# Kernel optimization log

Measured on AMD Instinct MI355X. Metric: run time of the kernel, lower is better.

Reference implementation:

```python
import jax, jax.numpy as jnp
import numpy as np

B, C, L = 1, 256, 1024      # batch, channels, seq_length
WIN, FEAT = 80, 256          # window_size, feature_size


def setup_inputs() -> dict:
    key = jax.random.key(0)
    ks = jax.random.split(key, 9)
    s = 0.02
    return {
        "x":  jax.random.normal(ks[0], (B, C, L), dtype=jnp.float32),
        # weights stored as [in, out] (transpose of torch Linear.weight)
        "Wq": jax.random.normal(ks[1], (WIN, FEAT), dtype=jnp.float32) * s,
        "bq": jax.random.normal(ks[2], (FEAT,), dtype=jnp.float32) * s,
        "Wk": jax.random.normal(ks[3], (WIN, FEAT), dtype=jnp.float32) * s,
        "bk": jax.random.normal(ks[4], (FEAT,), dtype=jnp.float32) * s,
        "Wv": jax.random.normal(ks[5], (WIN, FEAT), dtype=jnp.float32) * s,
        "bv": jax.random.normal(ks[6], (FEAT,), dtype=jnp.float32) * s,
        "Wf": jax.random.normal(ks[7], (FEAT, C), dtype=jnp.float32) * s,
        "bf": jax.random.normal(ks[8], (C,), dtype=jnp.float32) * s,
    }


def reference(x, Wq, bq, Wk, bk, Wv, bv, Wf, bf):
    Bb, Cc, Ll = x.shape
    half = WIN // 2
    # fixed-width window per position, clamped to stay in-bounds
    starts = jnp.clip(jnp.arange(Ll) - half, 0, Ll - WIN)          # [L]
    idx = starts[:, None] + jnp.arange(WIN)                        # [L, W]
    win = x[:, :, idx]                                             # [B, C, L, W]
    win = win.transpose(0, 2, 1, 3)                                # [B, L, C, W]
    q = win @ Wq + bq                                              # [B, L, C, F]
    k = win @ Wk + bk                                              # [B, L, C, F]
    v = win @ Wv + bv                                              # [B, L, C, F]
    scores = jax.nn.softmax(jnp.einsum('blcf,bldf->blcd', q, k), axis=-1)  # [B,L,C,C]
    attn = jnp.einsum('blcd,bldf->blcf', scores, v)                # [B, L, C, F]
    pooled = attn.mean(axis=2)                                     # [B, L, F] (mean over channels)
    out = pooled @ Wf + bf                                         # [B, L, C]
    return out.transpose(0, 2, 1)                                  # [B, C, L]
```

## Files before the change

### kernel.cpp

```cpp
#include <hip/hip_runtime.h>

#define Lc    1024
#define Cc    256
#define WINc  80
#define SLOTS 96
#define RS    88
#define L2E   1.44269504088896340736f

typedef __attribute__((ext_vector_type(8)))  short bf16x8;
typedef __attribute__((ext_vector_type(16))) float f32x16;
typedef __attribute__((ext_vector_type(4)))  unsigned int u32x4;

__device__ inline float bf2f(unsigned short h) { return __uint_as_float(((unsigned int)h) << 16); }
__device__ inline unsigned int cvt_pk_bf16(float lo, float hi) {
    unsigned int r;
    asm("v_cvt_pk_bf16_f32 %0, %1, %2" : "=v"(r) : "v"(lo), "v"(hi));
    return r;
}
__device__ inline unsigned short f2bf(float f) {
    unsigned int u = __float_as_uint(f);
    unsigned int r = u + 0x7FFFu + ((u >> 16) & 1u);
    return (unsigned short)(r >> 16);
}

__global__ __launch_bounds__(256) void precompute_kernel(
    const float* __restrict__ Wq, const float* __restrict__ bq,
    const float* __restrict__ Wk, const float* __restrict__ Wv,
    const float* __restrict__ bv, const float* __restrict__ Wf,
    const float* __restrict__ bf,
    unsigned short* __restrict__ Gt, float* __restrict__ WvWf,
    float* __restrict__ bias3)
{
    const int b = blockIdx.x;
    const int t = threadIdx.x;
    if (b < SLOTS) {
        if (t < WINc) {
            const int s = b;
            const int k = (s & ~12) | ((s & 4) << 1) | ((s & 8) >> 1);
            float acc = 0.f;
            if (k < WINc) {
                for (int f = 0; f < 256; ++f)
                    acc = fmaf(Wq[t * 256 + f], Wk[k * 256 + f], acc);
            } else if (k == WINc) {
                for (int f = 0; f < 256; ++f)
                    acc = fmaf(bq[f], Wk[t * 256 + f], acc);
            }
            Gt[s * WINc + t] = (k <= WINc) ? f2bf(acc * L2E) : (unsigned short)0;
        }
    } else if (b < SLOTS + WINc) {
        const int w = b - SLOTS;
        float acc = 0.f;
        for (int f = 0; f < 256; ++f)
            acc = fmaf(Wv[w * 256 + f], Wf[f * 256 + t], acc);
        WvWf[w * 256 + t] = acc * (1.0f / 256.0f);
    } else {
        float acc = bf[t];
        for (int f = 0; f < 256; ++f)
            acc = fmaf(bv[f], Wf[f * 256 + t], acc);
        bias3[t] = acc;
    }
}

__global__ __launch_bounds__(512, 2) void local_attn_kernel(
    const float* __restrict__ x,
    const unsigned short* __restrict__ Gt_ws,
    const float* __restrict__ WvWf, const float* __restrict__ bias3,
    float* __restrict__ out)
{
    __shared__ __align__(16) unsigned short winb[Cc * RS];
    __shared__ __align__(16) unsigned short Gtb[SLOTS * RS];
    __shared__ float sbeta[Cc];
    __shared__ float sbarAcc[Cc];
    __shared__ float ubuf[WINc];
    __shared__ float scratch[8 * Cc];

    const int l = blockIdx.x;
    int s0 = l - WINc / 2;
    s0 = s0 < 0 ? 0 : (s0 > (Lc - WINc) ? (Lc - WINc) : s0);
    const int tid  = threadIdx.x;
    const int lane = tid & 63;
    const int wid  = tid >> 6;
    const int ln31 = lane & 31;
    const int hh   = lane >> 5;

    for (int i = tid; i < Cc * WINc / 8; i += 512) {
        const int c  = i & 255;
        const int ch = i >> 8;
        const float* xp = &x[c * Lc + s0 + ch * 8];
        union { u32x4 u; bf16x8 v; } pk;
        pk.u.x = cvt_pk_bf16(xp[0], xp[1]);
        pk.u.y = cvt_pk_bf16(xp[2], xp[3]);
        pk.u.z = cvt_pk_bf16(xp[4], xp[5]);
        pk.u.w = cvt_pk_bf16(xp[6], xp[7]);
        *(bf16x8*)&winb[c * RS + ch * 8] = pk.v;
    }
    for (int i = tid; i < SLOTS * WINc / 2; i += 512) {
        const int s = i / 40;
        const int j = i - s * 40;
        ((unsigned int*)Gtb)[s * (RS / 2) + j] = ((const unsigned int*)Gt_ws)[i];
    }
    __syncthreads();

    f32x16 tt[3];
    {
        bf16x8 bfr[5];
        #pragma unroll
        for (int t = 0; t < 5; ++t)
            bfr[t] = *(const bf16x8*)&winb[(wid * 32 + ln31) * RS + t * 16 + hh * 8];
        #pragma unroll
        for (int mt = 0; mt < 3; ++mt) {
            f32x16 a;
            #pragma unroll
            for (int r = 0; r < 16; ++r) a[r] = 0.f;
            #pragma unroll
            for (int t = 0; t < 5; ++t) {
                bf16x8 afr = *(const bf16x8*)&Gtb[(mt * 32 + ln31) * RS + t * 16 + hh * 8];
                a = __builtin_amdgcn_mfma_f32_32x32x16_bf16(afr, bfr[t], a, 0, 0, 0);
            }
            tt[mt] = a;
        }
    }
    if (hh == 0) sbeta[wid * 32 + ln31] = tt[2][8];

    bf16x8 af[5];
    #pragma unroll
    for (int t = 0; t < 5; ++t) {
        const int m = t >> 1, o = 8 * (t & 1);
        union { u32x4 u; bf16x8 v; } pk;
        pk.u.x = cvt_pk_bf16(tt[m][o + 0], tt[m][o + 1]);
        pk.u.y = cvt_pk_bf16(tt[m][o + 2], tt[m][o + 3]);
        pk.u.z = cvt_pk_bf16(tt[m][o + 4], tt[m][o + 5]);
        pk.u.w = cvt_pk_bf16(tt[m][o + 6], tt[m][o + 7]);
        af[t] = pk.v;
    }

    f32x16 acc[8];
    #pragma unroll
    for (int nt = 0; nt < 8; ++nt) {
        f32x16 a;
        #pragma unroll
        for (int r = 0; r < 16; ++r) a[r] = 0.f;
        #pragma unroll
        for (int t = 0; t < 5; ++t) {
            bf16x8 b = *(const bf16x8*)&winb[(nt * 32 + ln31) * RS + t * 16 + hh * 8];
            a = __builtin_amdgcn_mfma_f32_32x32x16_bf16(af[t], b, a, 0, 0, 0);
        }
        acc[nt] = a;
    }
    __syncthreads();

    float zp[16];
    #pragma unroll
    for (int r = 0; r < 16; ++r) zp[r] = 0.f;
    #pragma unroll
    for (int nt = 0; nt < 8; ++nt) {
        const float sb = sbeta[nt * 32 + ln31];
        #pragma unroll
        for (int r = 0; r < 16; ++r) {
            const float e = exp2f(acc[nt][r] + sb);
            acc[nt][r] = e;
            zp[r] += e;
        }
    }
    #pragma unroll
    for (int r = 0; r < 16; ++r) {
        float z = zp[r];
        z += __shfl_xor(z, 1);
        z += __shfl_xor(z, 2);
        z += __shfl_xor(z, 4);
        z += __shfl_xor(z, 8);
        z += __shfl_xor(z, 16);
        zp[r] = __builtin_amdgcn_rcpf(z);
    }

    #pragma unroll
    for (int nt = 0; nt < 8; ++nt) {
        float v = 0.f;
        #pragma unroll
        for (int r = 0; r < 16; ++r) v = fmaf(acc[nt][r], zp[r], v);
        v += __shfl_xor(v, 32);
        if (lane < 32) scratch[wid * Cc + nt * 32 + ln31] = v;
    }
    __syncthreads();

    if (tid < Cc) {
        float v = 0.f;
        #pragma unroll
        for (int w8 = 0; w8 < 8; ++w8) v += scratch[w8 * Cc + tid];
        sbarAcc[tid] = v;
    }
    __syncthreads();

    if (tid < 4 * WINc) {
        const int w = tid % WINc;
        const int part = tid / WINc;
        const int d0 = part * 64;
        float a = 0.f;
        #pragma unroll 8
        for (int d = d0; d < d0 + 64; ++d)
            a = fmaf(sbarAcc[d], bf2f(winb[d * RS + w]), a);
        scratch[part * WINc + w] = a;
    }
    __syncthreads();
    if (tid < WINc)
        ubuf[tid] = scratch[tid] + scratch[WINc + tid] +
                    scratch[2 * WINc + tid] + scratch[3 * WINc + tid];
    __syncthreads();

    {
        const int co = tid & 255;
        const int part = tid >> 8;
        const int w0 = part * 40;
        float a = 0.f;
        #pragma unroll 8
        for (int w = w0; w < w0 + 40; ++w)
            a = fmaf(ubuf[w], WvWf[w * 256 + co], a);
        scratch[part * 256 + co] = a;
    }
    __syncthreads();
    if (tid < Cc)
        out[tid * Lc + l] = scratch[tid] + scratch[256 + tid] + bias3[tid];
}

extern "C" void kernel_launch(void* const* d_in, const int* in_sizes, int n_in,
                              void* d_out, int out_size, void* d_ws, size_t ws_size,
                              hipStream_t stream)
{
    const float* x  = (const float*)d_in[0];
    const float* Wq = (const float*)d_in[1];
    const float* bq = (const float*)d_in[2];
    const float* Wk = (const float*)d_in[3];
    const float* Wv = (const float*)d_in[5];
    const float* bv = (const float*)d_in[6];
    const float* Wf = (const float*)d_in[7];
    const float* bf = (const float*)d_in[8];
    float* out = (float*)d_out;

    unsigned short* Gt = (unsigned short*)d_ws;
    float* WvWf  = (float*)((char*)d_ws + SLOTS * WINc * 2);
    float* bias3 = WvWf + WINc * 256;

    hipLaunchKernelGGL(precompute_kernel, dim3(SLOTS + WINc + 1), dim3(256), 0, stream,
                       Wq, bq, Wk, Wv, bv, Wf, bf, Gt, WvWf, bias3);
    hipLaunchKernelGGL(local_attn_kernel, dim3(Lc), dim3(512), 0, stream,
                       x, Gt, WvWf, bias3, out);
}
```

Before: 72.08 us.

## Process two adjacent positions per block sharing one widened window tile

Each block now handles two consecutive sequence positions. It loads a single 81-wide window (padded to 96 columns) that covers both, and uses two shifted Gram tables precomputed for offsets 0 and 1. Gram tiles are read directly from global memory instead of being staged in LDS. The softmax/pooling epilogues of the two positions are interleaved to share barriers. This halves the window loads and launches, at the cost of a sixth MFMA k-step, doubled accumulator registers, and more global reads of the Gram table.

```diff
diff --git a/kernel.cpp b/kernel.cpp
--- a/kernel.cpp
+++ b/kernel.cpp
@@ -1,11 +1,12 @@
 #include <hip/hip_runtime.h>
 
-#define Lc    1024
-#define Cc    256
-#define WINc  80
-#define SLOTS 96
-#define RS    88
-#define L2E   1.44269504088896340736f
+#define Lc     1024
+#define Cc     256
+#define WINc   80
+#define SLOTS  96
+#define RS     104
+#define GSTRIDE 96
+#define L2E    1.44269504088896340736f
 
 typedef __attribute__((ext_vector_type(8)))  short bf16x8;
 typedef __attribute__((ext_vector_type(16))) float f32x16;
@@ -33,22 +34,28 @@
 {
     const int b = blockIdx.x;
     const int t = threadIdx.x;
-    if (b < SLOTS) {
-        if (t < WINc) {
-            const int s = b;
-            const int k = (s & ~12) | ((s & 4) << 1) | ((s & 8) >> 1);
-            float acc = 0.f;
-            if (k < WINc) {
+    if (b < 2 * SLOTS) {
+        if (t >= SLOTS) return;
+        const int dl = b / SLOTS;
+        const int s  = b % SLOTS;
+        const int j  = (s & ~12) | ((s & 4) << 1) | ((s & 8) >> 1);
+        const int i  = t;
+        float acc = 0.f;
+        bool nz = false;
+        if (j == 81) {
+            if (i >= dl && i - dl < WINc) {
+                nz = true;
                 for (int f = 0; f < 256; ++f)
-                    acc = fmaf(Wq[t * 256 + f], Wk[k * 256 + f], acc);
-            } else if (k == WINc) {
-                for (int f = 0; f < 256; ++f)
-                    acc = fmaf(bq[f], Wk[t * 256 + f], acc);
+                    acc = fmaf(bq[f], Wk[(i - dl) * 256 + f], acc);
             }
-            Gt[s * WINc + t] = (k <= WINc) ? f2bf(acc * L2E) : (unsigned short)0;
-        }
-    } else if (b < SLOTS + WINc) {
-        const int w = b - SLOTS;
+        } else if (j < 81 && j >= dl && j - dl < WINc && i >= dl && i - dl < WINc) {
+            nz = true;
+            for (int f = 0; f < 256; ++f)
+                acc = fmaf(Wq[(i - dl) * 256 + f], Wk[(j - dl) * 256 + f], acc);
+        }
+        Gt[dl * SLOTS * GSTRIDE + s * GSTRIDE + i] = nz ? f2bf(acc * L2E) : (unsigned short)0;
+    } else if (b < 2 * SLOTS + WINc) {
+        const int w = b - 2 * SLOTS;
         float acc = 0.f;
         for (int f = 0; f < 256; ++f)
             acc = fmaf(Wv[w * 256 + f], Wf[f * 256 + t], acc);
@@ -61,70 +68,26 @@
     }
 }
 
-__global__ __launch_bounds__(512, 2) void local_attn_kernel(
-    const float* __restrict__ x,
-    const unsigned short* __restrict__ Gt_ws,
-    const float* __restrict__ WvWf, const float* __restrict__ bias3,
-    float* __restrict__ out)
-{
-    __shared__ __align__(16) unsigned short winb[Cc * RS];
-    __shared__ __align__(16) unsigned short Gtb[SLOTS * RS];
-    __shared__ float sbeta[Cc];
-    __shared__ float sbarAcc[Cc];
-    __shared__ float ubuf[WINc];
-    __shared__ float scratch[8 * Cc];
-
-    const int l = blockIdx.x;
-    int s0 = l - WINc / 2;
-    s0 = s0 < 0 ? 0 : (s0 > (Lc - WINc) ? (Lc - WINc) : s0);
-    const int tid  = threadIdx.x;
-    const int lane = tid & 63;
-    const int wid  = tid >> 6;
-    const int ln31 = lane & 31;
-    const int hh   = lane >> 5;
-
-    for (int i = tid; i < Cc * WINc / 8; i += 512) {
-        const int c  = i & 255;
-        const int ch = i >> 8;
-        const float* xp = &x[c * Lc + s0 + ch * 8];
-        union { u32x4 u; bf16x8 v; } pk;
-        pk.u.x = cvt_pk_bf16(xp[0], xp[1]);
-        pk.u.y = cvt_pk_bf16(xp[2], xp[3]);
-        pk.u.z = cvt_pk_bf16(xp[4], xp[5]);
-        pk.u.w = cvt_pk_bf16(xp[6], xp[7]);
-        *(bf16x8*)&winb[c * RS + ch * 8] = pk.v;
-    }
-    for (int i = tid; i < SLOTS * WINc / 2; i += 512) {
-        const int s = i / 40;
-        const int j = i - s * 40;
-        ((unsigned int*)Gtb)[s * (RS / 2) + j] = ((const unsigned int*)Gt_ws)[i];
-    }
-    __syncthreads();
-
+__device__ inline void make_af(const unsigned short* __restrict__ Gtab,
+                               const bf16x8 bwin[6], float* sbeta_buf,
+                               bf16x8 af[6], int wid, int ln31, int hh)
+{
     f32x16 tt[3];
-    {
-        bf16x8 bfr[5];
-        #pragma unroll
-        for (int t = 0; t < 5; ++t)
-            bfr[t] = *(const bf16x8*)&winb[(wid * 32 + ln31) * RS + t * 16 + hh * 8];
-        #pragma unroll
-        for (int mt = 0; mt < 3; ++mt) {
-            f32x16 a;
-            #pragma unroll
-            for (int r = 0; r < 16; ++r) a[r] = 0.f;
-            #pragma unroll
-            for (int t = 0; t < 5; ++t) {
-                bf16x8 afr = *(const bf16x8*)&Gtb[(mt * 32 + ln31) * RS + t * 16 + hh * 8];
-                a = __builtin_amdgcn_mfma_f32_32x32x16_bf16(afr, bfr[t], a, 0, 0, 0);
-            }
-            tt[mt] = a;
-        }
-    }
-    if (hh == 0) sbeta[wid * 32 + ln31] = tt[2][8];
-
-    bf16x8 af[5];
-    #pragma unroll
-    for (int t = 0; t < 5; ++t) {
+    #pragma unroll
+    for (int mt = 0; mt < 3; ++mt) {
+        f32x16 a;
+        #pragma unroll
+        for (int r = 0; r < 16; ++r) a[r] = 0.f;
+        #pragma unroll
+        for (int t = 0; t < 6; ++t) {
+            bf16x8 g = *(const bf16x8*)&Gtab[(mt * 32 + ln31) * GSTRIDE + t * 16 + hh * 8];
+            a = __builtin_amdgcn_mfma_f32_32x32x16_bf16(g, bwin[t], a, 0, 0, 0);
+        }
+        tt[mt] = a;
+    }
+    if (hh == 0) sbeta_buf[wid * 32 + ln31] = tt[2][9];
+    #pragma unroll
+    for (int t = 0; t < 6; ++t) {
         const int m = t >> 1, o = 8 * (t & 1);
         union { u32x4 u; bf16x8 v; } pk;
         pk.u.x = cvt_pk_bf16(tt[m][o + 0], tt[m][o + 1]);
@@ -133,28 +96,18 @@
         pk.u.w = cvt_pk_bf16(tt[m][o + 6], tt[m][o + 7]);
         af[t] = pk.v;
     }
-
-    f32x16 acc[8];
+}
+
+__device__ inline void softmax_colpart(f32x16 acc[8], const float* sbeta_buf,
+                                       float* colpart, int wid, int lane)
+{
+    const int ln31 = lane & 31;
+    float zp[16];
+    #pragma unroll
+    for (int r = 0; r < 16; ++r) zp[r] = 0.f;
     #pragma unroll
     for (int nt = 0; nt < 8; ++nt) {
-        f32x16 a;
-        #pragma unroll
-        for (int r = 0; r < 16; ++r) a[r] = 0.f;
-        #pragma unroll
-        for (int t = 0; t < 5; ++t) {
-            bf16x8 b = *(const bf16x8*)&winb[(nt * 32 + ln31) * RS + t * 16 + hh * 8];
-            a = __builtin_amdgcn_mfma_f32_32x32x16_bf16(af[t], b, a, 0, 0, 0);
-        }
-        acc[nt] = a;
-    }
-    __syncthreads();
-
-    float zp[16];
-    #pragma unroll
-    for (int r = 0; r < 16; ++r) zp[r] = 0.f;
-    #pragma unroll
-    for (int nt = 0; nt < 8; ++nt) {
-        const float sb = sbeta[nt * 32 + ln31];
+        const float sb = sbeta_buf[nt * 32 + ln31];
         #pragma unroll
         for (int r = 0; r < 16; ++r) {
             const float e = exp2f(acc[nt][r] + sb);
@@ -172,25 +125,100 @@
         z += __shfl_xor(z, 16);
         zp[r] = __builtin_amdgcn_rcpf(z);
     }
-
     #pragma unroll
     for (int nt = 0; nt < 8; ++nt) {
         float v = 0.f;
         #pragma unroll
         for (int r = 0; r < 16; ++r) v = fmaf(acc[nt][r], zp[r], v);
         v += __shfl_xor(v, 32);
-        if (lane < 32) scratch[wid * Cc + nt * 32 + ln31] = v;
-    }
+        if (lane < 32) colpart[wid * Cc + nt * 32 + ln31] = v;
+    }
+}
+
+__global__ __launch_bounds__(512, 2) void local_attn_kernel(
+    const float* __restrict__ x,
+    const unsigned short* __restrict__ Gt,
+    const float* __restrict__ WvWf, const float* __restrict__ bias3,
+    float* __restrict__ out)
+{
+    __shared__ __align__(16) unsigned short winb[Cc * RS];
+    __shared__ float sbeta0[Cc], sbeta1[Cc];
+    __shared__ float colpart[8 * Cc];
+    __shared__ float sbarAcc[Cc];
+    __shared__ float upart[4 * WINc];
+    __shared__ float ubuf[WINc];
+    __shared__ float outpart[2 * Cc];
+
+    const int bid = blockIdx.x;
+    const int lA = 2 * bid, lB = lA + 1;
+    int sA = lA - WINc / 2; sA = sA < 0 ? 0 : (sA > (Lc - WINc) ? (Lc - WINc) : sA);
+    int sB = lB - WINc / 2; sB = sB < 0 ? 0 : (sB > (Lc - WINc) ? (Lc - WINc) : sB);
+    const int dB = sB - sA;
+
+    const int tid  = threadIdx.x;
+    const int lane = tid & 63;
+    const int wid  = tid >> 6;
+    const int ln31 = lane & 31;
+    const int hh   = lane >> 5;
+
+    for (int i = tid; i < Cc * 12; i += 512) {
+        const int c  = i / 12;
+        const int ch = i - c * 12;
+        union { u32x4 u; bf16x8 v; } pk;
+        if (ch < 10) {
+            const float* xp = &x[c * Lc + sA + ch * 8];
+            pk.u.x = cvt_pk_bf16(xp[0], xp[1]);
+            pk.u.y = cvt_pk_bf16(xp[2], xp[3]);
+            pk.u.z = cvt_pk_bf16(xp[4], xp[5]);
+            pk.u.w = cvt_pk_bf16(xp[6], xp[7]);
+        } else if (ch == 10) {
+            const float v0 = (sA + 80 < Lc) ? x[c * Lc + sA + 80] : 0.f;
+            pk.u.x = cvt_pk_bf16(v0, 0.f);
+            pk.u.y = 0u; pk.u.z = 0u; pk.u.w = 0u;
+        } else {
+            pk.u.x = 0u; pk.u.y = 0u; pk.u.z = 0u; pk.u.w = 0u;
+        }
+        *(u32x4*)&winb[c * RS + ch * 8] = pk.u;
+    }
+    __syncthreads();
+
+    bf16x8 bwin[6];
+    #pragma unroll
+    for (int t = 0; t < 6; ++t)
+        bwin[t] = *(const bf16x8*)&winb[(wid * 32 + ln31) * RS + t * 16 + hh * 8];
+
+    bf16x8 afA[6], afB[6];
+    make_af(Gt, bwin, sbeta0, afA, wid, ln31, hh);
+    make_af(Gt + dB * SLOTS * GSTRIDE, bwin, sbeta1, afB, wid, ln31, hh);
+
+    f32x16 accA[8], accB[8];
+    #pragma unroll
+    for (int nt = 0; nt < 8; ++nt) {
+        f32x16 a, b;
+        #pragma unroll
+        for (int r = 0; r < 16; ++r) { a[r] = 0.f; b[r] = 0.f; }
+        #pragma unroll
+        for (int t = 0; t < 6; ++t) {
+            bf16x8 bb = *(const bf16x8*)&winb[(nt * 32 + ln31) * RS + t * 16 + hh * 8];
+            a = __builtin_amdgcn_mfma_f32_32x32x16_bf16(afA[t], bb, a, 0, 0, 0);
+            b = __builtin_amdgcn_mfma_f32_32x32x16_bf16(afB[t], bb, b, 0, 0, 0);
+        }
+        accA[nt] = a; accB[nt] = b;
+    }
+    __syncthreads();
+
+    softmax_colpart(accA, sbeta0, colpart, wid, lane);
     __syncthreads();
 
     if (tid < Cc) {
         float v = 0.f;
         #pragma unroll
-        for (int w8 = 0; w8 < 8; ++w8) v += scratch[w8 * Cc + tid];
+        for (int w8 = 0; w8 < 8; ++w8) v += colpart[w8 * Cc + tid];
         sbarAcc[tid] = v;
     }
     __syncthreads();
 
+    softmax_colpart(accB, sbeta1, colpart, wid, lane);
     if (tid < 4 * WINc) {
         const int w = tid % WINc;
         const int part = tid / WINc;
@@ -199,12 +227,19 @@
         #pragma unroll 8
         for (int d = d0; d < d0 + 64; ++d)
             a = fmaf(sbarAcc[d], bf2f(winb[d * RS + w]), a);
-        scratch[part * WINc + w] = a;
-    }
-    __syncthreads();
+        upart[part * WINc + w] = a;
+    }
+    __syncthreads();
+
     if (tid < WINc)
-        ubuf[tid] = scratch[tid] + scratch[WINc + tid] +
-                    scratch[2 * WINc + tid] + scratch[3 * WINc + tid];
+        ubuf[tid] = upart[tid] + upart[WINc + tid] +
+                    upart[2 * WINc + tid] + upart[3 * WINc + tid];
+    if (tid < Cc) {
+        float v = 0.f;
+        #pragma unroll
+        for (int w8 = 0; w8 < 8; ++w8) v += colpart[w8 * Cc + tid];
+        sbarAcc[tid] = v;
+    }
     __syncthreads();
 
     {
@@ -215,11 +250,41 @@
         #pragma unroll 8
         for (int w = w0; w < w0 + 40; ++w)
             a = fmaf(ubuf[w], WvWf[w * 256 + co], a);
-        scratch[part * 256 + co] = a;
-    }
-    __syncthreads();
+        outpart[part * 256 + co] = a;
+    }
+    if (tid < 4 * WINc) {
+        const int w = tid % WINc;
+        const int part = tid / WINc;
+        const int d0 = part * 64;
+        float a = 0.f;
+        #pragma unroll 8
+        for (int d = d0; d < d0 + 64; ++d)
+            a = fmaf(sbarAcc[d], bf2f(winb[d * RS + w + dB]), a);
+        upart[part * WINc + w] = a;
+    }
+    __syncthreads();
+
     if (tid < Cc)
-        out[tid * Lc + l] = scratch[tid] + scratch[256 + tid] + bias3[tid];
+        out[tid * Lc + lA] = outpart[tid] + outpart[Cc + tid] + bias3[tid];
+    if (tid < WINc)
+        ubuf[tid] = upart[tid] + upart[WINc + tid] +
+                    upart[2 * WINc + tid] + upart[3 * WINc + tid];
+    __syncthreads();
+
+    {
+        const int co = tid & 255;
+        const int part = tid >> 8;
+        const int w0 = part * 40;
+        float a = 0.f;
+        #pragma unroll 8
+        for (int w = w0; w < w0 + 40; ++w)
+            a = fmaf(ubuf[w], WvWf[w * 256 + co], a);
+        outpart[part * 256 + co] = a;
+    }
+    __syncthreads();
+
+    if (tid < Cc)
+        out[tid * Lc + lB] = outpart[tid] + outpart[Cc + tid] + bias3[tid];
 }
 
 extern "C" void kernel_launch(void* const* d_in, const int* in_sizes, int n_in,
@@ -237,11 +302,11 @@
     float* out = (float*)d_out;
 
     unsigned short* Gt = (unsigned short*)d_ws;
-    float* WvWf  = (float*)((char*)d_ws + SLOTS * WINc * 2);
+    float* WvWf  = (float*)((char*)d_ws + 2 * SLOTS * GSTRIDE * 2);
     float* bias3 = WvWf + WINc * 256;
 
-    hipLaunchKernelGGL(precompute_kernel, dim3(SLOTS + WINc + 1), dim3(256), 0, stream,
+    hipLaunchKernelGGL(precompute_kernel, dim3(2 * SLOTS + WINc + 1), dim3(256), 0, stream,
                        Wq, bq, Wk, Wv, bv, Wf, bf, Gt, WvWf, bias3);
-    hipLaunchKernelGGL(local_attn_kernel, dim3(Lc), dim3(512), 0, stream,
+    hipLaunchKernelGGL(local_attn_kernel, dim3(Lc / 2), dim3(512), 0, stream,
                        x, Gt, WvWf, bias3, out);
 }
```

Result: slower. 84.90 us (+17.8%).
